# Optimization experiments

Measured on AMD Instinct MI355X. Metric: run time of the kernel, lower is better.

Reference implementation:

```python
import jax, jax.numpy as jnp
import numpy as np

NUM_USERS = 100000
NUM_ITEMS = 50000
EMBED_DIM = 64
NUM_LAYERS = 3
NUM_EDGES = 2000000
N = NUM_USERS + NUM_ITEMS


def setup_inputs() -> dict:
    key = jax.random.key(0)
    k_u, k_i, k_e = jax.random.split(key, 3)
    # Xavier-uniform init like nn.init.xavier_uniform_ on [num, dim]
    bound_u = float(np.sqrt(6.0 / (NUM_USERS + EMBED_DIM)))
    bound_i = float(np.sqrt(6.0 / (NUM_ITEMS + EMBED_DIM)))
    user_weight = jax.random.uniform(k_u, (NUM_USERS, EMBED_DIM), jnp.float32, -bound_u, bound_u)
    item_weight = jax.random.uniform(k_i, (NUM_ITEMS, EMBED_DIM), jnp.float32, -bound_i, bound_i)
    edge_index = jax.random.randint(k_e, (2, NUM_EDGES), 0, N, dtype=jnp.int64)
    return {"edge_index": edge_index, "user_weight": user_weight, "item_weight": item_weight}


def _propagate(x, row, col):
    # deg[v] = number of edges with col == v (in-degree of destination)
    deg = jax.ops.segment_sum(jnp.ones((row.shape[0],), x.dtype), col, num_segments=N)
    deg_inv = jnp.where(deg > 0, 1.0 / deg, 0.0)
    # gather messages from source nodes, scatter-add into destinations
    out = jax.ops.segment_sum(x[row], col, num_segments=N)  # [N, D]
    return out * deg_inv[:, None]


def reference(edge_index, user_weight, item_weight):
    row, col = edge_index[0], edge_index[1]
    x = jnp.concatenate([user_weight, item_weight], axis=0)  # [N, D]
    acc = x
    h = x
    for _ in range(NUM_LAYERS):
        h = _propagate(h, row, col)
        acc = acc + h
    final = acc / (NUM_LAYERS + 1)  # mean over layer outputs (incl. layer 0)
    return final[:NUM_USERS], final[NUM_USERS:]
```

## Files before the change

### kernel.cpp

```cpp
#include <hip/hip_runtime.h>

#define NUM_USERS 100000
#define NUM_ITEMS 50000
#define EMBED_DIM 64
#define NUM_EDGES 2000000
#define N_NODES   (NUM_USERS + NUM_ITEMS)

#define CAP         44
#define NSLICE      8
#define SLICE_CHUNK ((N_NODES + NSLICE - 1) / NSLICE)

__device__ __forceinline__ float bf_lo(unsigned u) { return __uint_as_float(u << 16); }
__device__ __forceinline__ float bf_hi(unsigned u) { return __uint_as_float(u & 0xffff0000u); }
__device__ __forceinline__ unsigned f2bf(float f) {
    unsigned u = __float_as_uint(f);
    u += 0x7fffu + ((u >> 16) & 1u);
    return u >> 16;
}
__device__ __forceinline__ unsigned pack2bf(float a, float b) {
    return f2bf(a) | (f2bf(b) << 16);
}

__global__ void fill_bucket_kernel(const int* __restrict__ row,
                                   const int* __restrict__ col,
                                   int* __restrict__ cur,
                                   int* __restrict__ bucket,
                                   const float* __restrict__ uw,
                                   const float* __restrict__ iw,
                                   unsigned* __restrict__ xbf) {
    const int gtid = blockIdx.x * blockDim.x + threadIdx.x;
    const int gstride = gridDim.x * blockDim.x;
    const long long totalU = (long long)N_NODES * EMBED_DIM / 2;
    const long long userU  = (long long)NUM_USERS * EMBED_DIM / 2;
    const float2* u2 = (const float2*)uw;
    const float2* i2 = (const float2*)iw;
    for (long long i = gtid; i < totalU; i += gstride) {
        float2 v = (i < userU) ? u2[i] : i2[i - userU];
        xbf[i] = pack2bf(v.x, v.y);
    }

    const int slice = blockIdx.x & (NSLICE - 1);
    const int rank  = blockIdx.x >> 3;
    const int nrank = gridDim.x >> 3;
    const int lo = slice * SLICE_CHUNK;
    const int hi = lo + SLICE_CHUNK;
    const int tid = rank * blockDim.x + threadIdx.x;
    const int stride = nrank * blockDim.x;
    const int4* col4 = (const int4*)col;
    const int4* row4 = (const int4*)row;
    const int n4 = NUM_EDGES / 4;
    for (int i = tid; i < n4; i += stride) {
        int4 c = col4[i];
        int4 r = row4[i];
        if (c.x >= lo && c.x < hi) {
            int s = atomicAdd(&cur[c.x], 1);
            if (s < CAP) bucket[c.x * CAP + s] = r.x;
        }
        if (c.y >= lo && c.y < hi) {
            int s = atomicAdd(&cur[c.y], 1);
            if (s < CAP) bucket[c.y * CAP + s] = r.y;
        }
        if (c.z >= lo && c.z < hi) {
            int s = atomicAdd(&cur[c.z], 1);
            if (s < CAP) bucket[c.z * CAP + s] = r.z;
        }
        if (c.w >= lo && c.w < hi) {
            int s = atomicAdd(&cur[c.w], 1);
            if (s < CAP) bucket[c.w * CAP + s] = r.w;
        }
    }
}

template <int MODE>
__global__ void gather_kernel(const int* __restrict__ degArr,
                              const int* __restrict__ bucket,
                              const unsigned short* __restrict__ src,
                              const unsigned short* __restrict__ h1,
                              const float* __restrict__ uw,
                              const float* __restrict__ iw,
                              unsigned short* __restrict__ dst_bf,
                              float* __restrict__ acc) {
    const int lane = threadIdx.x & 63;
    const int q    = lane >> 4;
    const int l16  = lane & 15;
    const int wave = (int)(((long long)blockIdx.x * blockDim.x + threadIdx.x) >> 6);
    const int nwaves = (gridDim.x * blockDim.x) >> 6;
    for (int v = wave; v < N_NODES; v += nwaves) {
        const int deg  = degArr[v];
        const int degc = (deg < CAP) ? deg : CAP;
        const int* b = bucket + (size_t)v * CAP;
        float4 s = make_float4(0.f, 0.f, 0.f, 0.f);
        int e = 0;
        for (; e + 8 <= degc; e += 8) {
            int ra = b[e + q];
            int rb = b[e + 4 + q];
            uint2 ua = *(const uint2*)(src + (size_t)ra * EMBED_DIM + l16 * 4);
            uint2 ub = *(const uint2*)(src + (size_t)rb * EMBED_DIM + l16 * 4);
            s.x += bf_lo(ua.x) + bf_lo(ub.x);
            s.y += bf_hi(ua.x) + bf_hi(ub.x);
            s.z += bf_lo(ua.y) + bf_lo(ub.y);
            s.w += bf_hi(ua.y) + bf_hi(ub.y);
        }
        for (; e + 4 <= degc; e += 4) {
            int r = b[e + q];
            uint2 u = *(const uint2*)(src + (size_t)r * EMBED_DIM + l16 * 4);
            s.x += bf_lo(u.x); s.y += bf_hi(u.x);
            s.z += bf_lo(u.y); s.w += bf_hi(u.y);
        }
        if (e + q < degc) {
            int r = b[e + q];
            uint2 u = *(const uint2*)(src + (size_t)r * EMBED_DIM + l16 * 4);
            s.x += bf_lo(u.x); s.y += bf_hi(u.x);
            s.z += bf_lo(u.y); s.w += bf_hi(u.y);
        }
        s.x += __shfl_xor(s.x, 16, 64); s.y += __shfl_xor(s.y, 16, 64);
        s.z += __shfl_xor(s.z, 16, 64); s.w += __shfl_xor(s.w, 16, 64);
        s.x += __shfl_xor(s.x, 32, 64); s.y += __shfl_xor(s.y, 32, 64);
        s.z += __shfl_xor(s.z, 32, 64); s.w += __shfl_xor(s.w, 32, 64);
        float dinv = (deg > 0) ? (1.0f / (float)deg) : 0.0f;
        if (q == 0) {
            float4 m = make_float4(s.x * dinv, s.y * dinv, s.z * dinv, s.w * dinv);
            size_t d = (size_t)l16 * 4;
            if (MODE < 2) {
                uint2 o;
                o.x = pack2bf(m.x, m.y);
                o.y = pack2bf(m.z, m.w);
                *(uint2*)(dst_bf + (size_t)v * EMBED_DIM + d) = o;
            } else {
                const float* xr = (v < NUM_USERS)
                    ? (uw + (size_t)v * EMBED_DIM)
                    : (iw + (size_t)(v - NUM_USERS) * EMBED_DIM);
                float4 x4 = *(const float4*)(xr + d);
                uint2 u1 = *(const uint2*)(h1 + (size_t)v * EMBED_DIM + d);
                uint2 u2 = *(const uint2*)(src + (size_t)v * EMBED_DIM + d);
                float4 a;
                a.x = 0.25f * (x4.x + bf_lo(u1.x) + bf_lo(u2.x) + m.x);
                a.y = 0.25f * (x4.y + bf_hi(u1.x) + bf_hi(u2.x) + m.y);
                a.z = 0.25f * (x4.z + bf_lo(u1.y) + bf_lo(u2.y) + m.z);
                a.w = 0.25f * (x4.w + bf_hi(u1.y) + bf_hi(u2.y) + m.w);
                *(float4*)(acc + (size_t)v * EMBED_DIM + d) = a;
            }
        }
    }
}

static inline size_t align4k(size_t x) { return (x + 4095) & ~(size_t)4095; }

extern "C" void kernel_launch(void* const* d_in, const int* in_sizes, int n_in,
                              void* d_out, int out_size, void* d_ws, size_t ws_size,
                              hipStream_t stream) {
    const int*   edges = (const int*)d_in[0];
    const float* uw    = (const float*)d_in[1];
    const float* iw    = (const float*)d_in[2];
    float* acc = (float*)d_out;

    const int* row = edges;
    const int* col = edges + NUM_EDGES;

    const size_t nodesI  = align4k((size_t)N_NODES * sizeof(int));
    const size_t bucketB = align4k((size_t)N_NODES * CAP * sizeof(int));
    const size_t matBF   = align4k((size_t)N_NODES * EMBED_DIM * 2);

    char* ws = (char*)d_ws;
    size_t o = 0;
    int*            cur    = (int*)(ws + o);            o += nodesI;
    int*            bucket = (int*)(ws + o);            o += bucketB;
    unsigned short* xbf    = (unsigned short*)(ws + o); o += matBF;
    unsigned short* h1     = (unsigned short*)(ws + o); o += matBF;
    unsigned short* h2     = (unsigned short*)(ws + o); o += matBF;

    hipMemsetAsync(cur, 0, (size_t)N_NODES * sizeof(int), stream);
    fill_bucket_kernel<<<2048, 256, 0, stream>>>(row, col, cur, bucket,
                                                 uw, iw, (unsigned*)xbf);

    gather_kernel<0><<<4096, 256, 0, stream>>>(cur, bucket, xbf, nullptr, uw, iw, h1, nullptr);
    gather_kernel<1><<<4096, 256, 0, stream>>>(cur, bucket, h1, nullptr, uw, iw, h2, nullptr);
    gather_kernel<2><<<4096, 256, 0, stream>>>(cur, bucket, h2, h1, uw, iw, nullptr, acc);
}
```

Baseline: 278.5 us.

## Replace global-atomic edge bucketing with binned radix partition and shared-memory fill

```diff
diff --git a/kernel.cpp b/kernel.cpp
--- a/kernel.cpp
+++ b/kernel.cpp
@@ -6,9 +6,15 @@
 #define NUM_EDGES 2000000
 #define N_NODES   (NUM_USERS + NUM_ITEMS)
 
-#define CAP         44
-#define NSLICE      8
-#define SLICE_CHUNK ((N_NODES + NSLICE - 1) / NSLICE)
+#define CAP       44
+#define BIN_SHIFT 9
+#define BIN_SIZE  (1 << BIN_SHIFT)
+#define NBIN      ((N_NODES + BIN_SIZE - 1) >> BIN_SHIFT)
+#define NBLK      512
+#define EDGES4    (NUM_EDGES / 4)
+#define CHUNK4    ((EDGES4 + NBLK - 1) / NBLK)
+#define SCAN_LEN  (NBIN * NBLK)
+#define NB_SCAN2  (SCAN_LEN / 256)
 
 __device__ __forceinline__ float bf_lo(unsigned u) { return __uint_as_float(u << 16); }
 __device__ __forceinline__ float bf_hi(unsigned u) { return __uint_as_float(u & 0xffff0000u); }
@@ -21,13 +27,30 @@
     return f2bf(a) | (f2bf(b) << 16);
 }
 
-__global__ void fill_bucket_kernel(const int* __restrict__ row,
-                                   const int* __restrict__ col,
-                                   int* __restrict__ cur,
-                                   int* __restrict__ bucket,
-                                   const float* __restrict__ uw,
-                                   const float* __restrict__ iw,
-                                   unsigned* __restrict__ xbf) {
+__global__ void hist_bf16_kernel(const int* __restrict__ col,
+                                 int* __restrict__ H,
+                                 const float* __restrict__ uw,
+                                 const float* __restrict__ iw,
+                                 unsigned* __restrict__ xbf) {
+    __shared__ int hist[NBIN];
+    for (int t = threadIdx.x; t < NBIN; t += blockDim.x) hist[t] = 0;
+    __syncthreads();
+
+    const int b  = blockIdx.x;
+    const int i0 = b * CHUNK4;
+    const int i1 = min(i0 + CHUNK4, EDGES4);
+    const int4* col4 = (const int4*)col;
+    for (int i = i0 + threadIdx.x; i < i1; i += blockDim.x) {
+        int4 c = col4[i];
+        atomicAdd(&hist[c.x >> BIN_SHIFT], 1);
+        atomicAdd(&hist[c.y >> BIN_SHIFT], 1);
+        atomicAdd(&hist[c.z >> BIN_SHIFT], 1);
+        atomicAdd(&hist[c.w >> BIN_SHIFT], 1);
+    }
+    __syncthreads();
+    for (int t = threadIdx.x; t < NBIN; t += blockDim.x)
+        H[b * NBIN + t] = hist[t];
+
     const int gtid = blockIdx.x * blockDim.x + threadIdx.x;
     const int gstride = gridDim.x * blockDim.x;
     const long long totalU = (long long)N_NODES * EMBED_DIM / 2;
@@ -38,37 +61,101 @@
         float2 v = (i < userU) ? u2[i] : i2[i - userU];
         xbf[i] = pack2bf(v.x, v.y);
     }
-
-    const int slice = blockIdx.x & (NSLICE - 1);
-    const int rank  = blockIdx.x >> 3;
-    const int nrank = gridDim.x >> 3;
-    const int lo = slice * SLICE_CHUNK;
-    const int hi = lo + SLICE_CHUNK;
-    const int tid = rank * blockDim.x + threadIdx.x;
-    const int stride = nrank * blockDim.x;
+}
+
+__global__ void block_scan_T_kernel(const int* __restrict__ H,
+                                    int* __restrict__ S,
+                                    int* __restrict__ blockSums) {
+    __shared__ int s[256];
+    int gid = blockIdx.x * 256 + threadIdx.x;
+    int blk = gid & (NBLK - 1);
+    int bin = gid >> 9;
+    int v = H[blk * NBIN + bin];
+    s[threadIdx.x] = v;
+    __syncthreads();
+    for (int o = 1; o < 256; o <<= 1) {
+        int t = (threadIdx.x >= o) ? s[threadIdx.x - o] : 0;
+        __syncthreads();
+        s[threadIdx.x] += t;
+        __syncthreads();
+    }
+    S[gid] = s[threadIdx.x] - v;
+    if (threadIdx.x == 255) blockSums[blockIdx.x] = s[255];
+}
+
+__global__ void scan_sums_kernel(int* __restrict__ blockSums, int nb) {
+    __shared__ int s[1024];
+    int v = (threadIdx.x < nb) ? blockSums[threadIdx.x] : 0;
+    s[threadIdx.x] = v;
+    __syncthreads();
+    for (int o = 1; o < 1024; o <<= 1) {
+        int t = ((int)threadIdx.x >= o) ? s[threadIdx.x - o] : 0;
+        __syncthreads();
+        s[threadIdx.x] += t;
+        __syncthreads();
+    }
+    if ((int)threadIdx.x < nb) blockSums[threadIdx.x] = s[threadIdx.x] - v;
+}
+
+__global__ void add_sums_kernel(int* __restrict__ S,
+                                const int* __restrict__ blockSums) {
+    int gid = blockIdx.x * 256 + threadIdx.x;
+    S[gid] += blockSums[blockIdx.x];
+}
+
+__global__ void partition_kernel(const int* __restrict__ row,
+                                 const int* __restrict__ col,
+                                 const int* __restrict__ S,
+                                 uint2* __restrict__ part) {
+    __shared__ int base[NBIN];
+    __shared__ int cur[NBIN];
+    const int b = blockIdx.x;
+    for (int t = threadIdx.x; t < NBIN; t += blockDim.x) {
+        base[t] = S[t * NBLK + b];
+        cur[t]  = 0;
+    }
+    __syncthreads();
+    const int i0 = b * CHUNK4;
+    const int i1 = min(i0 + CHUNK4, EDGES4);
     const int4* col4 = (const int4*)col;
     const int4* row4 = (const int4*)row;
-    const int n4 = NUM_EDGES / 4;
-    for (int i = tid; i < n4; i += stride) {
+    for (int i = i0 + threadIdx.x; i < i1; i += blockDim.x) {
         int4 c = col4[i];
         int4 r = row4[i];
-        if (c.x >= lo && c.x < hi) {
-            int s = atomicAdd(&cur[c.x], 1);
-            if (s < CAP) bucket[c.x * CAP + s] = r.x;
-        }
-        if (c.y >= lo && c.y < hi) {
-            int s = atomicAdd(&cur[c.y], 1);
-            if (s < CAP) bucket[c.y * CAP + s] = r.y;
-        }
-        if (c.z >= lo && c.z < hi) {
-            int s = atomicAdd(&cur[c.z], 1);
-            if (s < CAP) bucket[c.z * CAP + s] = r.z;
-        }
-        if (c.w >= lo && c.w < hi) {
-            int s = atomicAdd(&cur[c.w], 1);
-            if (s < CAP) bucket[c.w * CAP + s] = r.w;
-        }
-    }
+        int bn, p;
+        bn = c.x >> BIN_SHIFT; p = base[bn] + atomicAdd(&cur[bn], 1);
+        part[p] = make_uint2((unsigned)c.x, (unsigned)r.x);
+        bn = c.y >> BIN_SHIFT; p = base[bn] + atomicAdd(&cur[bn], 1);
+        part[p] = make_uint2((unsigned)c.y, (unsigned)r.y);
+        bn = c.z >> BIN_SHIFT; p = base[bn] + atomicAdd(&cur[bn], 1);
+        part[p] = make_uint2((unsigned)c.z, (unsigned)r.z);
+        bn = c.w >> BIN_SHIFT; p = base[bn] + atomicAdd(&cur[bn], 1);
+        part[p] = make_uint2((unsigned)c.w, (unsigned)r.w);
+    }
+}
+
+__global__ void bucket_fill_kernel(const int* __restrict__ S,
+                                   const uint2* __restrict__ part,
+                                   int* __restrict__ bucket,
+                                   int* __restrict__ deg) {
+    __shared__ int cur[BIN_SIZE];
+    const int bin = blockIdx.x;
+    cur[threadIdx.x] = 0;
+    cur[threadIdx.x + 256] = 0;
+    __syncthreads();
+    const int e0 = S[bin * NBLK];
+    const int e1 = (bin + 1 < NBIN) ? S[(bin + 1) * NBLK] : NUM_EDGES;
+    for (int e = e0 + threadIdx.x; e < e1; e += blockDim.x) {
+        uint2 pr = part[e];
+        int c = (int)pr.x;
+        int slot = atomicAdd(&cur[c & (BIN_SIZE - 1)], 1);
+        if (slot < CAP) bucket[(size_t)c * CAP + slot] = (int)pr.y;
+    }
+    __syncthreads();
+    int v0 = (bin << BIN_SHIFT) + threadIdx.x;
+    if (v0 < N_NODES) deg[v0] = cur[threadIdx.x];
+    int v1 = v0 + 256;
+    if (v1 < N_NODES) deg[v1] = cur[threadIdx.x + 256];
 }
 
 template <int MODE>
@@ -157,23 +244,35 @@
     const int* row = edges;
     const int* col = edges + NUM_EDGES;
 
-    const size_t nodesI  = align4k((size_t)N_NODES * sizeof(int));
+    const size_t scanB   = align4k((size_t)SCAN_LEN * sizeof(int));
+    const size_t bsumsB  = align4k((size_t)NB_SCAN2 * sizeof(int));
+    const size_t degB    = align4k((size_t)N_NODES * sizeof(int));
     const size_t bucketB = align4k((size_t)N_NODES * CAP * sizeof(int));
     const size_t matBF   = align4k((size_t)N_NODES * EMBED_DIM * 2);
 
     char* ws = (char*)d_ws;
     size_t o = 0;
-    int*            cur    = (int*)(ws + o);            o += nodesI;
+    int*            H      = (int*)(ws + o);            o += scanB;
+    int*            S      = (int*)(ws + o);            o += scanB;
+    int*            bsums  = (int*)(ws + o);            o += bsumsB;
+    int*            deg    = (int*)(ws + o);            o += degB;
     int*            bucket = (int*)(ws + o);            o += bucketB;
     unsigned short* xbf    = (unsigned short*)(ws + o); o += matBF;
     unsigned short* h1     = (unsigned short*)(ws + o); o += matBF;
     unsigned short* h2     = (unsigned short*)(ws + o); o += matBF;
-
-    hipMemsetAsync(cur, 0, (size_t)N_NODES * sizeof(int), stream);
-    fill_bucket_kernel<<<2048, 256, 0, stream>>>(row, col, cur, bucket,
-                                                 uw, iw, (unsigned*)xbf);
-
-    gather_kernel<0><<<4096, 256, 0, stream>>>(cur, bucket, xbf, nullptr, uw, iw, h1, nullptr);
-    gather_kernel<1><<<4096, 256, 0, stream>>>(cur, bucket, h1, nullptr, uw, iw, h2, nullptr);
-    gather_kernel<2><<<4096, 256, 0, stream>>>(cur, bucket, h2, h1, uw, iw, nullptr, acc);
-}
+    uint2* part = (uint2*)h1;
+
+    hist_bf16_kernel<<<NBLK, 256, 0, stream>>>(col, H, uw, iw, (unsigned*)xbf);
+
+    block_scan_T_kernel<<<NB_SCAN2, 256, 0, stream>>>(H, S, bsums);
+    scan_sums_kernel<<<1, 1024, 0, stream>>>(bsums, NB_SCAN2);
+    add_sums_kernel<<<NB_SCAN2, 256, 0, stream>>>(S, bsums);
+
+    partition_kernel<<<NBLK, 256, 0, stream>>>(row, col, S, part);
+
+    bucket_fill_kernel<<<NBIN, 256, 0, stream>>>(S, part, bucket, deg);
+
+    gather_kernel<0><<<4096, 256, 0, stream>>>(deg, bucket, xbf, nullptr, uw, iw, h1, nullptr);
+    gather_kernel<1><<<4096, 256, 0, stream>>>(deg, bucket, h1, nullptr, uw, iw, h2, nullptr);
+    gather_kernel<2><<<4096, 256, 0, stream>>>(deg, bucket, h2, h1, uw, iw, nullptr, acc);
+}
```

Result: faster. 229.0 us (-17.8%).
